# Optimization experiments

Hardware: AMD Instinct MI355X
Metric: run time of the kernel (lower is better)

Reference implementation:

```python
import jax, jax.numpy as jnp
import numpy as np
import math

# ---- HashGridEncoder constants (from init_kwargs) ----
L = 16            # levels
LOG2T = 19
T = 1 << LOG2T    # hash table size per level
F = 2             # features per entry
N_MIN = 16
N_MAX = 2048
N_PTS = 524288    # number of query points
BB_MIN = np.zeros(3, np.float32)
BB_MAX = np.ones(3, np.float32)
B = math.exp((math.log(N_MAX) - math.log(N_MIN)) / (L - 1))
RES = np.array([math.floor(N_MIN * B ** i) for i in range(L)], dtype=np.float32)  # per-level grid resolution
VERTS = np.array([[0,0,0],[0,0,1],[0,1,0],[0,1,1],[1,0,0],[1,0,1],[1,1,0],[1,1,1]], dtype=np.int32)  # 8 cube corners
PI = np.array([1, 2654435761, 805459861], dtype=np.uint32)  # spatial hash primes
MASK = np.uint32((1 << 19) - 1)  # hard-coded mask from source


def setup_inputs() -> dict:
    key = jax.random.key(0)
    k1, k2 = jax.random.split(key)
    xyz = jax.random.uniform(k1, (N_PTS, 3), dtype=jnp.float32)  # points inside bbox [0,1]^3
    # nn.init.uniform_(weight, -1e-4, 1e-4)
    tables = jax.random.uniform(k2, (L, T, F), minval=-1e-4, maxval=1e-4, dtype=jnp.float32)
    return {"xyz": xyz, "tables": tables}


def reference(xyz, tables):
    # cell size per level: (bb_max - bb_min) / resolution  -> [L,3]
    cell = (BB_MAX - BB_MIN)[None, :] / RES[:, None]
    # normalized grid coords for all levels at once: [L,N,3]
    u = (xyz[None, :, :] - BB_MIN) / cell[:, None, :]
    mi = jnp.floor(u).astype(jnp.int32)            # min corner index [L,N,3]
    d = u - mi.astype(jnp.float32)                 # trilinear fracs == (xyz - min_vertex)/cell, [L,N,3]
    # 8 corner integer coords: [L,N,8,3]; uint32 wrapping matches int64-mul + low-19-bit mask
    corners = (mi[:, :, None, :] + VERTS[None, None]).astype(jnp.uint32)
    h = (corners[..., 0] * PI[0]) ^ (corners[..., 1] * PI[1]) ^ (corners[..., 2] * PI[2])
    h = (h & MASK).astype(jnp.int32)               # hash indices [L,N,8], all < T
    # gather all levels in one flat lookup
    flat = tables.reshape(L * T, F)
    idx = h + (jnp.arange(L, dtype=jnp.int32) * T)[:, None, None]
    emb = flat[idx]                                # [L,N,8,F]
    # trilinear weights: prod over axes of d (corner bit 1) or 1-d (corner bit 0) -> [L,N,8]
    w = jnp.prod(jnp.where(VERTS[None, None].astype(bool), d[:, :, None, :], 1.0 - d[:, :, None, :]), axis=-1)
    c = jnp.einsum('lnv,lnvf->lnf', w, emb)        # interpolated features [L,N,F]
    # torch.cat(embedded, dim=-1): level-major concat -> [N, L*F]
    return jnp.moveaxis(c, 0, 1).reshape(xyz.shape[0], L * F)
```

## Files before the change

kernel.cpp:

```cpp
#include <hip/hip_runtime.h>
#include <cmath>

#define NLEVELS 16
#define HMASK   0x7FFFFu
#define NPTS    524288
#define NBUCKET 32768

typedef float v4f __attribute__((ext_vector_type(4)));

struct LevelParams {
    float cell[NLEVELS];
};

__device__ __forceinline__ unsigned spread5(unsigned v) {
    return (v & 1u) | ((v & 2u) << 2) | ((v & 4u) << 4) |
           ((v & 8u) << 6) | ((v & 16u) << 8);
}

__device__ __forceinline__ unsigned morton_key(float x, float y, float z) {
    unsigned bx = min(31u, (unsigned)(x * 32.0f));
    unsigned by = min(31u, (unsigned)(y * 32.0f));
    unsigned bz = min(31u, (unsigned)(z * 32.0f));
    return spread5(bx) | (spread5(by) << 1) | (spread5(bz) << 2);
}

__device__ __forceinline__ void ngp_hash(
    float x, float y, float z, float cell, unsigned* __restrict__ h,
    float& dx, float& dy, float& dz)
{
    const float ux = x / cell;
    const float uy = y / cell;
    const float uz = z / cell;
    const float fx = floorf(ux);
    const float fy = floorf(uy);
    const float fz = floorf(uz);
    dx = ux - fx;
    dy = uy - fy;
    dz = uz - fz;

    const unsigned ix = (unsigned)(int)fx;
    const unsigned iy = (unsigned)(int)fy;
    const unsigned iz = (unsigned)(int)fz;

    const unsigned hx0 = ix;
    const unsigned hx1 = ix + 1u;
    const unsigned hy0 = iy * 2654435761u;
    const unsigned hy1 = (iy + 1u) * 2654435761u;
    const unsigned hz0 = iz * 805459861u;
    const unsigned hz1 = (iz + 1u) * 805459861u;

    h[0] = (hx0 ^ hy0 ^ hz0) & HMASK;
    h[1] = (hx0 ^ hy0 ^ hz1) & HMASK;
    h[2] = (hx0 ^ hy1 ^ hz0) & HMASK;
    h[3] = (hx0 ^ hy1 ^ hz1) & HMASK;
    h[4] = (hx1 ^ hy0 ^ hz0) & HMASK;
    h[5] = (hx1 ^ hy0 ^ hz1) & HMASK;
    h[6] = (hx1 ^ hy1 ^ hz0) & HMASK;
    h[7] = (hx1 ^ hy1 ^ hz1) & HMASK;
}

__device__ __forceinline__ void ngp_weights(
    float dx, float dy, float dz, float* __restrict__ w)
{
    const float wx0 = 1.0f - dx;
    const float wy0 = 1.0f - dy;
    const float wz0 = 1.0f - dz;
    const float p00 = wx0 * wy0;
    const float p01 = wx0 * dy;
    const float p10 = dx * wy0;
    const float p11 = dx * dy;
    w[0] = p00 * wz0;
    w[1] = p00 * dz;
    w[2] = p01 * wz0;
    w[3] = p01 * dz;
    w[4] = p10 * wz0;
    w[5] = p10 * dz;
    w[6] = p11 * wz0;
    w[7] = p11 * dz;
}

__device__ __forceinline__ float2 ngp_combine(
    const float* __restrict__ w, const float2* __restrict__ e)
{
    float c0 = w[0] * e[0].x;
    float c1 = w[0] * e[0].y;
    #pragma unroll
    for (int c = 1; c < 8; ++c) {
        c0 += w[c] * e[c].x;
        c1 += w[c] * e[c].y;
    }
    return make_float2(c0, c1);
}

__global__ __launch_bounds__(256) void bucket_count(
    const float* __restrict__ xyz, unsigned* __restrict__ counts)
{
    const int n = blockIdx.x * 256 + threadIdx.x;
    const float x = xyz[3 * n + 0];
    const float y = xyz[3 * n + 1];
    const float z = xyz[3 * n + 2];
    atomicAdd(&counts[morton_key(x, y, z)], 1u);
}

__global__ __launch_bounds__(1024) void bucket_scan(
    const unsigned* __restrict__ counts, unsigned* __restrict__ cursor)
{
    __shared__ unsigned psum[1024];
    const unsigned t = threadIdx.x;

    unsigned s = 0;
    for (int i = 0; i < 32; ++i) s += counts[t * 32 + i];
    psum[t] = s;
    __syncthreads();

    for (unsigned off = 1; off < 1024; off <<= 1) {
        unsigned v = 0;
        if (t >= off) v = psum[t - off];
        __syncthreads();
        if (t >= off) psum[t] += v;
        __syncthreads();
    }

    unsigned excl = psum[t] - s;
    for (int i = 0; i < 32; ++i) {
        cursor[t * 32 + i] = excl;
        excl += counts[t * 32 + i];
    }
}

__global__ __launch_bounds__(256) void bucket_scatter(
    const float* __restrict__ xyz, unsigned* __restrict__ cursor,
    unsigned* __restrict__ perm, float* __restrict__ xyz_sorted)
{
    const int n = blockIdx.x * 256 + threadIdx.x;
    const float x = xyz[3 * n + 0];
    const float y = xyz[3 * n + 1];
    const float z = xyz[3 * n + 2];
    const unsigned key = morton_key(x, y, z);
    const unsigned p = atomicAdd(&cursor[key], 1u);
    perm[p] = (unsigned)n;
    xyz_sorted[3 * p + 0] = x;
    xyz_sorted[3 * p + 1] = y;
    xyz_sorted[3 * p + 2] = z;
}

__global__ __launch_bounds__(256) void ngp_phase1(
    const float* __restrict__ xyz_sorted,
    const float* __restrict__ tables,
    float2* __restrict__ ws,
    LevelParams lp)
{
    const unsigned b = blockIdx.x;
    const int level = (int)(b >> 11);
    const int chunk = (int)(b & 2047u);
    const int p = chunk * 256 + threadIdx.x;

    const float x = xyz_sorted[3 * p + 0];
    const float y = xyz_sorted[3 * p + 1];
    const float z = xyz_sorted[3 * p + 2];

    const float cell = lp.cell[level];
    const float2* __restrict__ tab = (const float2*)tables + ((size_t)level << 19);

    unsigned h[8];
    float dx, dy, dz;
    ngp_hash(x, y, z, cell, h, dx, dy, dz);

    float2 e[8];
    #pragma unroll
    for (int c = 0; c < 8; ++c) e[c] = tab[h[c]];

    float w[8];
    ngp_weights(dx, dy, dz, w);

    const float2 r = ngp_combine(w, e);

    ws[(size_t)level * NPTS + p] = r;
}

#define P2S 257

__global__ __launch_bounds__(256) void ngp_phase2(
    const float2* __restrict__ ws,
    const unsigned* __restrict__ perm,
    float* __restrict__ out)
{
    __shared__ float2 lds[NLEVELS * P2S];
    __shared__ unsigned nperm[256];
    const unsigned base = blockIdx.x * 256;
    const unsigned t = threadIdx.x;

    nperm[t] = perm[base + t];
    #pragma unroll
    for (int l = 0; l < NLEVELS; ++l)
        lds[l * P2S + t] = ws[(size_t)l * NPTS + base + t];

    __syncthreads();

    #pragma unroll
    for (int it = 0; it < 8; ++it) {
        const unsigned j = it * 256 + t;
        const unsigned pl = j >> 3;
        const unsigned k = j & 7u;
        const float2 a = lds[(2u * k)      * P2S + pl];
        const float2 b = lds[(2u * k + 1u) * P2S + pl];
        v4f v = { a.x, a.y, b.x, b.y };
        *(v4f*)(out + (size_t)nperm[pl] * 32 + k * 4) = v;
    }
}

__global__ __launch_bounds__(256) void ngp_encode(
    const float* __restrict__ xyz,
    const float* __restrict__ tables,
    float* __restrict__ out,
    LevelParams lp)
{
    const int n = blockIdx.x * 256 + threadIdx.x;
    const float x = xyz[3 * n + 0];
    const float y = xyz[3 * n + 1];
    const float z = xyz[3 * n + 2];

    float acc[2 * NLEVELS];
    const float2* __restrict__ tab_base = (const float2*)tables;

    #pragma unroll
    for (int l = 0; l < NLEVELS; ++l) {
        unsigned h[8];
        float dx, dy, dz;
        ngp_hash(x, y, z, lp.cell[l], h, dx, dy, dz);
        const float2* __restrict__ tab = tab_base + ((size_t)l << 19);
        float2 e[8];
        #pragma unroll
        for (int c = 0; c < 8; ++c) e[c] = tab[h[c]];
        float w[8];
        ngp_weights(dx, dy, dz, w);
        const float2 r = ngp_combine(w, e);
        acc[2 * l + 0] = r.x;
        acc[2 * l + 1] = r.y;
    }

    v4f* o4 = (v4f*)(out + (size_t)n * 32);
    #pragma unroll
    for (int j = 0; j < 8; ++j) {
        v4f v = { acc[4 * j + 0], acc[4 * j + 1],
                  acc[4 * j + 2], acc[4 * j + 3] };
        o4[j] = v;
    }
}

extern "C" void kernel_launch(void* const* d_in, const int* in_sizes, int n_in,
                              void* d_out, int out_size, void* d_ws, size_t ws_size,
                              hipStream_t stream) {
    const float* xyz    = (const float*)d_in[0];
    const float* tables = (const float*)d_in[1];
    float* out          = (float*)d_out;

    LevelParams lp;
    const double B = std::exp((std::log(2048.0) - std::log(16.0)) / 15.0);
    for (int i = 0; i < NLEVELS; ++i) {
        const double r = std::floor(16.0 * std::pow(B, (double)i));
        lp.cell[i] = 1.0f / (float)r;
    }

    const size_t off_feat   = 0;
    const size_t off_xyzs   = off_feat + (size_t)NLEVELS * NPTS * sizeof(float2);
    const size_t off_perm   = off_xyzs + (size_t)NPTS * 3 * sizeof(float);
    const size_t off_counts = off_perm + (size_t)NPTS * sizeof(unsigned);
    const size_t off_cursor = off_counts + (size_t)NBUCKET * sizeof(unsigned);
    const size_t ws_needed  = off_cursor + (size_t)NBUCKET * sizeof(unsigned);

    if (ws_size >= ws_needed) {
        char* wsb = (char*)d_ws;
        float2*   ws_feat    = (float2*)(wsb + off_feat);
        float*    xyz_sorted = (float*)(wsb + off_xyzs);
        unsigned* perm       = (unsigned*)(wsb + off_perm);
        unsigned* counts     = (unsigned*)(wsb + off_counts);
        unsigned* cursor     = (unsigned*)(wsb + off_cursor);

        hipMemsetAsync(counts, 0, NBUCKET * sizeof(unsigned), stream);
        hipLaunchKernelGGL(bucket_count, dim3(NPTS / 256), dim3(256), 0, stream,
                           xyz, counts);
        hipLaunchKernelGGL(bucket_scan, dim3(1), dim3(1024), 0, stream,
                           counts, cursor);
        hipLaunchKernelGGL(bucket_scatter, dim3(NPTS / 256), dim3(256), 0, stream,
                           xyz, cursor, perm, xyz_sorted);
        hipLaunchKernelGGL(ngp_phase1, dim3(NLEVELS * (NPTS / 256)), dim3(256), 0, stream,
                           xyz_sorted, tables, ws_feat, lp);
        hipLaunchKernelGGL(ngp_phase2, dim3(NPTS / 256), dim3(256), 0, stream,
                           ws_feat, perm, out);
    } else {
        hipLaunchKernelGGL(ngp_encode, dim3(NPTS / 256), dim3(256), 0, stream,
                           xyz, tables, out, lp);
    }
}
```

Baseline: 357.4 us.

## Pack sorted points with index, stage scan in LDS, add cache hints on gathers

Several changes land at once. Sorted xyz and the permutation index are merged into one 16-byte record so each point is a single vector load. The bucket scan is staged through a swizzled LDS buffer so global accesses coalesce. Fine-level table gathers use inline asm loads with the sc0 cache hint, and the intermediate and output stores use nontemporal hints. These aim to cut memory traffic and cache pollution, but the inline asm forces a full wait before the weight maths and may limit overlap.

```diff
diff --git a/kernel.cpp b/kernel.cpp
--- a/kernel.cpp
+++ b/kernel.cpp
@@ -7,6 +7,7 @@
 #define NBUCKET 32768
 
 typedef float v4f __attribute__((ext_vector_type(4)));
+typedef float v2f __attribute__((ext_vector_type(2)));
 
 struct LevelParams {
     float cell[NLEVELS];
@@ -79,8 +80,8 @@
     w[7] = p11 * dz;
 }
 
-__device__ __forceinline__ float2 ngp_combine(
-    const float* __restrict__ w, const float2* __restrict__ e)
+__device__ __forceinline__ v2f ngp_combine(
+    const float* __restrict__ w, const v2f* __restrict__ e)
 {
     float c0 = w[0] * e[0].x;
     float c1 = w[0] * e[0].y;
@@ -89,7 +90,8 @@
         c0 += w[c] * e[c].x;
         c1 += w[c] * e[c].y;
     }
-    return make_float2(c0, c1);
+    v2f r = { c0, c1 };
+    return r;
 }
 
 __global__ __launch_bounds__(256) void bucket_count(
@@ -105,11 +107,23 @@
 __global__ __launch_bounds__(1024) void bucket_scan(
     const unsigned* __restrict__ counts, unsigned* __restrict__ cursor)
 {
+    __shared__ unsigned c[NBUCKET];
     __shared__ unsigned psum[1024];
     const unsigned t = threadIdx.x;
 
+    #pragma unroll
+    for (int i = 0; i < 32; ++i) {
+        const unsigned idx = (unsigned)i * 1024u + t;
+        c[idx ^ ((idx >> 5) & 31u)] = counts[idx];
+    }
+    __syncthreads();
+
     unsigned s = 0;
-    for (int i = 0; i < 32; ++i) s += counts[t * 32 + i];
+    #pragma unroll
+    for (int i = 0; i < 32; ++i) {
+        const unsigned idx = t * 32u + (unsigned)i;
+        s += c[idx ^ ((idx >> 5) & 31u)];
+    }
     psum[t] = s;
     __syncthreads();
 
@@ -122,15 +136,26 @@
     }
 
     unsigned excl = psum[t] - s;
+    #pragma unroll
     for (int i = 0; i < 32; ++i) {
-        cursor[t * 32 + i] = excl;
-        excl += counts[t * 32 + i];
+        const unsigned idx = t * 32u + (unsigned)i;
+        const unsigned sw  = idx ^ ((idx >> 5) & 31u);
+        const unsigned v = c[sw];
+        c[sw] = excl;
+        excl += v;
+    }
+    __syncthreads();
+
+    #pragma unroll
+    for (int i = 0; i < 32; ++i) {
+        const unsigned idx = (unsigned)i * 1024u + t;
+        cursor[idx] = c[idx ^ ((idx >> 5) & 31u)];
     }
 }
 
 __global__ __launch_bounds__(256) void bucket_scatter(
     const float* __restrict__ xyz, unsigned* __restrict__ cursor,
-    unsigned* __restrict__ perm, float* __restrict__ xyz_sorted)
+    v4f* __restrict__ pts)
 {
     const int n = blockIdx.x * 256 + threadIdx.x;
     const float x = xyz[3 * n + 0];
@@ -138,16 +163,14 @@
     const float z = xyz[3 * n + 2];
     const unsigned key = morton_key(x, y, z);
     const unsigned p = atomicAdd(&cursor[key], 1u);
-    perm[p] = (unsigned)n;
-    xyz_sorted[3 * p + 0] = x;
-    xyz_sorted[3 * p + 1] = y;
-    xyz_sorted[3 * p + 2] = z;
+    v4f v = { x, y, z, __uint_as_float((unsigned)n) };
+    pts[p] = v;
 }
 
 __global__ __launch_bounds__(256) void ngp_phase1(
-    const float* __restrict__ xyz_sorted,
+    const v4f* __restrict__ pts,
     const float* __restrict__ tables,
-    float2* __restrict__ ws,
+    v2f* __restrict__ ws,
     LevelParams lp)
 {
     const unsigned b = blockIdx.x;
@@ -155,45 +178,72 @@
     const int chunk = (int)(b & 2047u);
     const int p = chunk * 256 + threadIdx.x;
 
-    const float x = xyz_sorted[3 * p + 0];
-    const float y = xyz_sorted[3 * p + 1];
-    const float z = xyz_sorted[3 * p + 2];
+    const v4f q = pts[p];
 
     const float cell = lp.cell[level];
-    const float2* __restrict__ tab = (const float2*)tables + ((size_t)level << 19);
+    const v2f* __restrict__ tab = (const v2f*)tables + ((size_t)level << 19);
 
     unsigned h[8];
     float dx, dy, dz;
-    ngp_hash(x, y, z, cell, h, dx, dy, dz);
-
-    float2 e[8];
-    #pragma unroll
-    for (int c = 0; c < 8; ++c) e[c] = tab[h[c]];
+    ngp_hash(q.x, q.y, q.z, cell, h, dx, dy, dz);
+
+    v2f e[8];
+    if (level >= 7) {
+        v2f e0, e1, e2, e3, e4, e5, e6, e7;
+        const v2f* a0 = tab + h[0];
+        const v2f* a1 = tab + h[1];
+        const v2f* a2 = tab + h[2];
+        const v2f* a3 = tab + h[3];
+        const v2f* a4 = tab + h[4];
+        const v2f* a5 = tab + h[5];
+        const v2f* a6 = tab + h[6];
+        const v2f* a7 = tab + h[7];
+        asm volatile(
+            "global_load_dwordx2 %0, %8, off sc0\n\t"
+            "global_load_dwordx2 %1, %9, off sc0\n\t"
+            "global_load_dwordx2 %2, %10, off sc0\n\t"
+            "global_load_dwordx2 %3, %11, off sc0\n\t"
+            "global_load_dwordx2 %4, %12, off sc0\n\t"
+            "global_load_dwordx2 %5, %13, off sc0\n\t"
+            "global_load_dwordx2 %6, %14, off sc0\n\t"
+            "global_load_dwordx2 %7, %15, off sc0\n\t"
+            "s_waitcnt vmcnt(0)"
+            : "=&v"(e0), "=&v"(e1), "=&v"(e2), "=&v"(e3),
+              "=&v"(e4), "=&v"(e5), "=&v"(e6), "=&v"(e7)
+            : "v"(a0), "v"(a1), "v"(a2), "v"(a3),
+              "v"(a4), "v"(a5), "v"(a6), "v"(a7));
+        e[0] = e0; e[1] = e1; e[2] = e2; e[3] = e3;
+        e[4] = e4; e[5] = e5; e[6] = e6; e[7] = e7;
+    } else {
+        #pragma unroll
+        for (int c = 0; c < 8; ++c) e[c] = tab[h[c]];
+    }
 
     float w[8];
     ngp_weights(dx, dy, dz, w);
 
-    const float2 r = ngp_combine(w, e);
-
-    ws[(size_t)level * NPTS + p] = r;
+    const v2f r = ngp_combine(w, e);
+
+    __builtin_nontemporal_store(r, &ws[(size_t)level * NPTS + p]);
 }
 
 #define P2S 257
 
 __global__ __launch_bounds__(256) void ngp_phase2(
-    const float2* __restrict__ ws,
-    const unsigned* __restrict__ perm,
+    const v2f* __restrict__ ws,
+    const v4f* __restrict__ pts,
     float* __restrict__ out)
 {
-    __shared__ float2 lds[NLEVELS * P2S];
+    __shared__ v2f lds[NLEVELS * P2S];
     __shared__ unsigned nperm[256];
     const unsigned base = blockIdx.x * 256;
     const unsigned t = threadIdx.x;
 
-    nperm[t] = perm[base + t];
+    nperm[t] = __float_as_uint(pts[base + t].w);
     #pragma unroll
     for (int l = 0; l < NLEVELS; ++l)
-        lds[l * P2S + t] = ws[(size_t)l * NPTS + base + t];
+        lds[l * P2S + t] =
+            __builtin_nontemporal_load(&ws[(size_t)l * NPTS + base + t]);
 
     __syncthreads();
 
@@ -202,10 +252,11 @@
         const unsigned j = it * 256 + t;
         const unsigned pl = j >> 3;
         const unsigned k = j & 7u;
-        const float2 a = lds[(2u * k)      * P2S + pl];
-        const float2 b = lds[(2u * k + 1u) * P2S + pl];
+        const v2f a = lds[(2u * k)      * P2S + pl];
+        const v2f b = lds[(2u * k + 1u) * P2S + pl];
         v4f v = { a.x, a.y, b.x, b.y };
-        *(v4f*)(out + (size_t)nperm[pl] * 32 + k * 4) = v;
+        __builtin_nontemporal_store(
+            v, (v4f*)(out + (size_t)nperm[pl] * 32 + k * 4));
     }
 }
 
@@ -221,20 +272,20 @@
     const float z = xyz[3 * n + 2];
 
     float acc[2 * NLEVELS];
-    const float2* __restrict__ tab_base = (const float2*)tables;
+    const v2f* __restrict__ tab_base = (const v2f*)tables;
 
     #pragma unroll
     for (int l = 0; l < NLEVELS; ++l) {
         unsigned h[8];
         float dx, dy, dz;
         ngp_hash(x, y, z, lp.cell[l], h, dx, dy, dz);
-        const float2* __restrict__ tab = tab_base + ((size_t)l << 19);
-        float2 e[8];
+        const v2f* __restrict__ tab = tab_base + ((size_t)l << 19);
+        v2f e[8];
         #pragma unroll
         for (int c = 0; c < 8; ++c) e[c] = tab[h[c]];
         float w[8];
         ngp_weights(dx, dy, dz, w);
-        const float2 r = ngp_combine(w, e);
+        const v2f r = ngp_combine(w, e);
         acc[2 * l + 0] = r.x;
         acc[2 * l + 1] = r.y;
     }
@@ -263,19 +314,17 @@
     }
 
     const size_t off_feat   = 0;
-    const size_t off_xyzs   = off_feat + (size_t)NLEVELS * NPTS * sizeof(float2);
-    const size_t off_perm   = off_xyzs + (size_t)NPTS * 3 * sizeof(float);
-    const size_t off_counts = off_perm + (size_t)NPTS * sizeof(unsigned);
+    const size_t off_pts    = off_feat + (size_t)NLEVELS * NPTS * sizeof(v2f);
+    const size_t off_counts = off_pts + (size_t)NPTS * sizeof(v4f);
     const size_t off_cursor = off_counts + (size_t)NBUCKET * sizeof(unsigned);
     const size_t ws_needed  = off_cursor + (size_t)NBUCKET * sizeof(unsigned);
 
     if (ws_size >= ws_needed) {
         char* wsb = (char*)d_ws;
-        float2*   ws_feat    = (float2*)(wsb + off_feat);
-        float*    xyz_sorted = (float*)(wsb + off_xyzs);
-        unsigned* perm       = (unsigned*)(wsb + off_perm);
-        unsigned* counts     = (unsigned*)(wsb + off_counts);
-        unsigned* cursor     = (unsigned*)(wsb + off_cursor);
+        v2f*      ws_feat = (v2f*)(wsb + off_feat);
+        v4f*      pts     = (v4f*)(wsb + off_pts);
+        unsigned* counts  = (unsigned*)(wsb + off_counts);
+        unsigned* cursor  = (unsigned*)(wsb + off_cursor);
 
         hipMemsetAsync(counts, 0, NBUCKET * sizeof(unsigned), stream);
         hipLaunchKernelGGL(bucket_count, dim3(NPTS / 256), dim3(256), 0, stream,
@@ -283,11 +332,11 @@
         hipLaunchKernelGGL(bucket_scan, dim3(1), dim3(1024), 0, stream,
                            counts, cursor);
         hipLaunchKernelGGL(bucket_scatter, dim3(NPTS / 256), dim3(256), 0, stream,
-                           xyz, cursor, perm, xyz_sorted);
+                           xyz, cursor, pts);
         hipLaunchKernelGGL(ngp_phase1, dim3(NLEVELS * (NPTS / 256)), dim3(256), 0, stream,
-                           xyz_sorted, tables, ws_feat, lp);
+                           pts, tables, ws_feat, lp);
         hipLaunchKernelGGL(ngp_phase2, dim3(NPTS / 256), dim3(256), 0, stream,
-                           ws_feat, perm, out);
+                           ws_feat, pts, out);
     } else {
         hipLaunchKernelGGL(ngp_encode, dim3(NPTS / 256), dim3(256), 0, stream,
                            xyz, tables, out, lp);
```

After: 351.1 us. About the same (-1.8%).
